# Optimization experiments

Measured on AMD Instinct MI355X. Metric: run time of the kernel, lower is better.

## Reference

```python
import jax, jax.numpy as jnp
import numpy as np

N_NODES = 50000
N_EDGES = 800000
D = 128


def setup_inputs() -> dict:
    key = jax.random.key(0)
    k1, k2, k3, k4, k5 = jax.random.split(key, 5)
    node_attr = jax.random.normal(k1, (N_NODES, D), dtype=jnp.float32)
    edge_index = jax.random.randint(k2, (2, N_EDGES), 0, N_NODES, dtype=jnp.int64)
    edge_attr = jax.random.normal(k3, (N_EDGES, D), dtype=jnp.float32)
    # 2-layer MLP: (3D -> D) -> ReLU -> (D -> D), scaled init
    w1 = jax.random.normal(k4, (3 * D, D), dtype=jnp.float32) * (1.0 / np.sqrt(3 * D))
    b1 = jnp.zeros((D,), dtype=jnp.float32)
    w2 = jax.random.normal(k5, (D, D), dtype=jnp.float32) * (1.0 / np.sqrt(D))
    b2 = jnp.zeros((D,), dtype=jnp.float32)
    return {"node_attr": node_attr, "edge_index": edge_index, "edge_attr": edge_attr,
            "w1": w1, "b1": b1, "w2": w2, "b2": b2}


def reference(node_attr, edge_index, edge_attr, w1, b1, w2, b2):
    senders_idx = edge_index[0]
    receivers_idx = edge_index[1]
    senders_attr = node_attr[senders_idx]      # [E, D] irregular gather
    receivers_attr = node_attr[receivers_idx]  # [E, D] irregular gather
    collected = jnp.concatenate([senders_attr, receivers_attr, edge_attr], axis=1)  # [E, 3D]
    h = jax.nn.relu(collected @ w1 + b1)       # [E, D]
    edge_attr_new = h @ w2 + b2                # [E, D]
    return edge_attr_new
```

## Files before the change

### kernel.cpp

```cpp
#include <hip/hip_runtime.h>


#define NE 800000
#define DD 128

typedef float f32x4v __attribute__((ext_vector_type(4)));
typedef float f32x16 __attribute__((ext_vector_type(16)));
typedef _Float16 f16x8 __attribute__((ext_vector_type(8)));
typedef _Float16 f16x4 __attribute__((ext_vector_type(4)));

__device__ __forceinline__ f16x4 cvt4(f32x4v v) {
    f16x4 r;
    r[0] = (_Float16)v[0]; r[1] = (_Float16)v[1];
    r[2] = (_Float16)v[2]; r[3] = (_Float16)v[3];
    return r;
}

__global__ void prep_w(const float* __restrict__ w1, const float* __restrict__ w2,
                       _Float16* __restrict__ w1t, _Float16* __restrict__ w2f) {
    int i = blockIdx.x * 256 + threadIdx.x;
    if (i < 384 * 128) {
        int col = i / 384;
        int k = i - col * 384;
        float v = w1[(size_t)k * 128 + col];
        int byteoff = col * 768 + ((k * 2) ^ ((col & 15) << 4));
        *(_Float16*)((char*)w1t + byteoff) = (_Float16)v;
    } else {
        int j = i - 384 * 128;
        int kk2 = j >> 10;
        int col = (j >> 3) & 127;
        int jj = j & 7;
        w2f[j] = (_Float16)w2[(size_t)(kk2 * 8 + jj) * 128 + col];
    }
}

#define MFMA_SEG(SEG)                                                                     \
    _Pragma("unroll")                                                                     \
    for (int kk8 = 0; kk8 < 8; kk8++) {                                                   \
        f16x8 a = *(const f16x8*)(ab + r31 * 256 + ((kk8 * 32 + g2 * 16) ^ xa));          \
        _Pragma("unroll")                                                                 \
        for (int n = 0; n < 4; n++) {                                                     \
            const int col = n * 32 + r31;                                                 \
            f16x8 b = *(const f16x8*)(lds + col * 768 +                                   \
                       ((((SEG) * 8 + kk8) * 32 + g2 * 16) ^ ((col & 15) << 4)));         \
            acc[n] = __builtin_amdgcn_mfma_f32_32x32x16_f16(a, b, acc[n], 0, 0, 0);       \
        }                                                                                 \
    }

#define WRITE_SEG(V)                                                                      \
    _Pragma("unroll")                                                                     \
    for (int i = 0; i < 16; i++) {                                                        \
        const int row = 2 * i + g2;                                                       \
        *(f16x4*)(ab + row * 256 + ((r31 * 8) ^ ((row & 15) << 4))) = cvt4(V[i]);         \
    }

__global__ __attribute__((amdgpu_flat_work_group_size(512, 512),
                          amdgpu_waves_per_eu(2, 2)))
void edge_mlp(
    const float* __restrict__ node_attr,
    const int* __restrict__ eidx,
    const float* __restrict__ edge_attr,
    const _Float16* __restrict__ w1t,
    const float* __restrict__ b1,
    const _Float16* __restrict__ w2f,
    const float* __restrict__ b2,
    float* __restrict__ out) {
    extern __shared__ char lds[];

    const int tid = threadIdx.x;
    const int wid = tid >> 6;
    const int lane = tid & 63;
    const int r31 = lane & 31;
    const int g2 = lane >> 5;

    {
        const char* src = (const char*)w1t;
        #pragma unroll
        for (int i = 0; i < 12; i++) {
            int off = (tid + i * 512) * 16;
            *(f16x8*)(lds + off) = *(const f16x8*)(src + off);
        }
    }

    float b1v[4], b2v[4];
    #pragma unroll
    for (int n = 0; n < 4; n++) { b1v[n] = b1[n * 32 + r31]; b2v[n] = b2[n * 32 + r31]; }

    __syncthreads();

    const int ebase = blockIdx.x * 256 + wid * 32;
    char* ab = lds + 96 * 1024 + wid * 8192;
    const int xa = (r31 & 15) << 4;

    const int sidx = eidx[ebase + r31];
    const int ridx = eidx[NE + ebase + r31];

    f32x4v sv[16];
    #pragma unroll
    for (int i = 0; i < 16; i++) {
        int r = __shfl(sidx, 2 * i + g2);
        sv[i] = *(const f32x4v*)(node_attr + (size_t)r * DD + r31 * 4);
    }
    __builtin_amdgcn_sched_barrier(0);

    WRITE_SEG(sv)

    f32x4v rv[16];
    #pragma unroll
    for (int i = 0; i < 16; i++) {
        int r = __shfl(ridx, 2 * i + g2);
        rv[i] = *(const f32x4v*)(node_attr + (size_t)r * DD + r31 * 4);
    }
    f32x4v ev[16];
    #pragma unroll
    for (int i = 0; i < 16; i++) {
        const int row = 2 * i + g2;
        ev[i] = __builtin_nontemporal_load(
            (const f32x4v*)(edge_attr + (size_t)(ebase + row) * DD + r31 * 4));
    }
    __builtin_amdgcn_sched_barrier(0);

    f32x16 acc[4] = {};
    __builtin_amdgcn_wave_barrier();

    MFMA_SEG(0)

    WRITE_SEG(rv)
    __builtin_amdgcn_wave_barrier();

    MFMA_SEG(1)

    WRITE_SEG(ev)

    f16x8 b2f[8][4];
    #pragma unroll
    for (int kk = 0; kk < 8; kk++)
        #pragma unroll
        for (int n = 0; n < 4; n++)
            b2f[kk][n] = *(const f16x8*)(w2f + ((size_t)((kk * 2 + g2) * 128 + n * 32 + r31)) * 8);
    __builtin_amdgcn_sched_barrier(0);
    __builtin_amdgcn_wave_barrier();

    MFMA_SEG(2)

    #pragma unroll
    for (int n = 0; n < 4; n++) {
        const int col = n * 32 + r31;
        #pragma unroll
        for (int reg = 0; reg < 16; reg++) {
            const int row = (reg & 3) + 8 * (reg >> 2) + 4 * g2;
            float v = fmaxf(acc[n][reg] + b1v[n], 0.0f);
            *(_Float16*)(ab + row * 256 + ((col * 2) ^ ((row & 15) << 4))) = (_Float16)v;
        }
    }
    __builtin_amdgcn_wave_barrier();

    f32x16 acc2[4] = {};
    #pragma unroll
    for (int kk = 0; kk < 8; kk++) {
        f16x8 a = *(const f16x8*)(ab + r31 * 256 + ((kk * 32 + g2 * 16) ^ xa));
        #pragma unroll
        for (int n = 0; n < 4; n++)
            acc2[n] = __builtin_amdgcn_mfma_f32_32x32x16_f16(a, b2f[kk][n], acc2[n], 0, 0, 0);
    }

    #pragma unroll
    for (int n = 0; n < 4; n++) {
        #pragma unroll
        for (int reg = 0; reg < 16; reg++) {
            const int row = (reg & 3) + 8 * (reg >> 2) + 4 * g2;
            __builtin_nontemporal_store(acc2[n][reg] + b2v[n],
                out + (size_t)(ebase + row) * DD + n * 32 + r31);
        }
    }
}

extern "C" void kernel_launch(void* const* d_in, const int* in_sizes, int n_in,
                              void* d_out, int out_size, void* d_ws, size_t ws_size,
                              hipStream_t stream) {
    const float* node_attr = (const float*)d_in[0];
    const int* eidx = (const int*)d_in[1];
    const float* edge_attr = (const float*)d_in[2];
    const float* w1 = (const float*)d_in[3];
    const float* b1 = (const float*)d_in[4];
    const float* w2 = (const float*)d_in[5];
    const float* b2 = (const float*)d_in[6];
    float* out = (float*)d_out;

    _Float16* w1t = (_Float16*)d_ws;
    _Float16* w2f = w1t + 384 * 128;

    hipFuncSetAttribute((const void*)edge_mlp,
                        hipFuncAttributeMaxDynamicSharedMemorySize, 160 * 1024);

    prep_w<<<256, 256, 0, stream>>>(w1, w2, w1t, w2f);
    edge_mlp<<<3125, 512, 160 * 1024, stream>>>(node_attr, eidx, edge_attr,
                                                w1t, b1, w2f, b2, out);
}
```

Before: 288.6 us.

## Make edge MLP kernel persistent with cross-tile prefetch of sender gathers

Launches 256 persistent blocks that loop over 32-edge wave tiles with a stride of 2048, so the W1 copy into LDS is paid once per block instead of once per 256 edges. Inside the loop, the next tile's edge indices and sender-row gathers are issued before the final MFMA segment, overlapping gather latency with compute. W2 fragments are now loaded in two halves per iteration rather than held whole, which lowers register pressure at the cost of repeated global/L2 reads. The risk is a less even load split across CUs and extra register use for the prefetched sender rows.

```diff
diff --git a/kernel.cpp b/kernel.cpp
--- a/kernel.cpp
+++ b/kernel.cpp
@@ -3,6 +3,8 @@
 
 #define NE 800000
 #define DD 128
+#define NWT 25000
+#define WSTRIDE 2048
 
 typedef float f32x4v __attribute__((ext_vector_type(4)));
 typedef float f32x16 __attribute__((ext_vector_type(16)));
@@ -88,14 +90,14 @@
 
     __syncthreads();
 
-    const int ebase = blockIdx.x * 256 + wid * 32;
     char* ab = lds + 96 * 1024 + wid * 8192;
     const int xa = (r31 & 15) << 4;
 
-    const int sidx = eidx[ebase + r31];
-    const int ridx = eidx[NE + ebase + r31];
-
-    f32x4v sv[16];
+    int g = blockIdx.x * 8 + wid;
+    int sidx = eidx[g * 32 + r31];
+    int ridx = eidx[NE + g * 32 + r31];
+
+    f32x4v sv[16], rv[16], ev[16];
     #pragma unroll
     for (int i = 0; i < 16; i++) {
         int r = __shfl(sidx, 2 * i + g2);
@@ -103,75 +105,104 @@
     }
     __builtin_amdgcn_sched_barrier(0);
 
-    WRITE_SEG(sv)
-
-    f32x4v rv[16];
-    #pragma unroll
-    for (int i = 0; i < 16; i++) {
-        int r = __shfl(ridx, 2 * i + g2);
-        rv[i] = *(const f32x4v*)(node_attr + (size_t)r * DD + r31 * 4);
-    }
-    f32x4v ev[16];
-    #pragma unroll
-    for (int i = 0; i < 16; i++) {
-        const int row = 2 * i + g2;
-        ev[i] = __builtin_nontemporal_load(
-            (const f32x4v*)(edge_attr + (size_t)(ebase + row) * DD + r31 * 4));
-    }
-    __builtin_amdgcn_sched_barrier(0);
-
-    f32x16 acc[4] = {};
-    __builtin_amdgcn_wave_barrier();
-
-    MFMA_SEG(0)
-
-    WRITE_SEG(rv)
-    __builtin_amdgcn_wave_barrier();
-
-    MFMA_SEG(1)
-
-    WRITE_SEG(ev)
-
-    f16x8 b2f[8][4];
-    #pragma unroll
-    for (int kk = 0; kk < 8; kk++)
-        #pragma unroll
-        for (int n = 0; n < 4; n++)
-            b2f[kk][n] = *(const f16x8*)(w2f + ((size_t)((kk * 2 + g2) * 128 + n * 32 + r31)) * 8);
-    __builtin_amdgcn_sched_barrier(0);
-    __builtin_amdgcn_wave_barrier();
-
-    MFMA_SEG(2)
-
-    #pragma unroll
-    for (int n = 0; n < 4; n++) {
-        const int col = n * 32 + r31;
-        #pragma unroll
-        for (int reg = 0; reg < 16; reg++) {
-            const int row = (reg & 3) + 8 * (reg >> 2) + 4 * g2;
-            float v = fmaxf(acc[n][reg] + b1v[n], 0.0f);
-            *(_Float16*)(ab + row * 256 + ((col * 2) ^ ((row & 15) << 4))) = (_Float16)v;
-        }
-    }
-    __builtin_amdgcn_wave_barrier();
-
-    f32x16 acc2[4] = {};
-    #pragma unroll
-    for (int kk = 0; kk < 8; kk++) {
-        f16x8 a = *(const f16x8*)(ab + r31 * 256 + ((kk * 32 + g2 * 16) ^ xa));
-        #pragma unroll
-        for (int n = 0; n < 4; n++)
-            acc2[n] = __builtin_amdgcn_mfma_f32_32x32x16_f16(a, b2f[kk][n], acc2[n], 0, 0, 0);
-    }
-
-    #pragma unroll
-    for (int n = 0; n < 4; n++) {
-        #pragma unroll
-        for (int reg = 0; reg < 16; reg++) {
-            const int row = (reg & 3) + 8 * (reg >> 2) + 4 * g2;
-            __builtin_nontemporal_store(acc2[n][reg] + b2v[n],
-                out + (size_t)(ebase + row) * DD + n * 32 + r31);
-        }
+    while (g < NWT) {
+        const int ebase = g * 32;
+
+        WRITE_SEG(sv)
+
+        #pragma unroll
+        for (int i = 0; i < 16; i++) {
+            int r = __shfl(ridx, 2 * i + g2);
+            rv[i] = *(const f32x4v*)(node_attr + (size_t)r * DD + r31 * 4);
+        }
+        #pragma unroll
+        for (int i = 0; i < 16; i++) {
+            const int row = 2 * i + g2;
+            ev[i] = __builtin_nontemporal_load(
+                (const f32x4v*)(edge_attr + (size_t)(ebase + row) * DD + r31 * 4));
+        }
+        __builtin_amdgcn_sched_barrier(0);
+
+        const int gn = g + WSTRIDE;
+        int sidx_n = 0, ridx_n = 0;
+        if (gn < NWT) {
+            sidx_n = eidx[gn * 32 + r31];
+            ridx_n = eidx[NE + gn * 32 + r31];
+        }
+
+        f32x16 acc[4] = {};
+        __builtin_amdgcn_wave_barrier();
+        MFMA_SEG(0)
+
+        WRITE_SEG(rv)
+        __builtin_amdgcn_wave_barrier();
+        MFMA_SEG(1)
+
+        WRITE_SEG(ev)
+        __builtin_amdgcn_wave_barrier();
+
+        if (gn < NWT) {
+            #pragma unroll
+            for (int i = 0; i < 16; i++) {
+                int r = __shfl(sidx_n, 2 * i + g2);
+                sv[i] = *(const f32x4v*)(node_attr + (size_t)r * DD + r31 * 4);
+            }
+        }
+        __builtin_amdgcn_sched_barrier(0);
+
+        MFMA_SEG(2)
+
+        #pragma unroll
+        for (int n = 0; n < 4; n++) {
+            const int col = n * 32 + r31;
+            #pragma unroll
+            for (int reg = 0; reg < 16; reg++) {
+                const int row = (reg & 3) + 8 * (reg >> 2) + 4 * g2;
+                float v = fmaxf(acc[n][reg] + b1v[n], 0.0f);
+                *(_Float16*)(ab + row * 256 + ((col * 2) ^ ((row & 15) << 4))) = (_Float16)v;
+            }
+        }
+        __builtin_amdgcn_wave_barrier();
+
+        f32x16 acc2[4] = {};
+        f16x8 b2fa[4][4];
+        #pragma unroll
+        for (int kk = 0; kk < 4; kk++)
+            #pragma unroll
+            for (int n = 0; n < 4; n++)
+                b2fa[kk][n] = *(const f16x8*)(w2f + ((size_t)((kk * 2 + g2) * 128 + n * 32 + r31)) * 8);
+        #pragma unroll
+        for (int kk = 0; kk < 4; kk++) {
+            f16x8 a = *(const f16x8*)(ab + r31 * 256 + ((kk * 32 + g2 * 16) ^ xa));
+            #pragma unroll
+            for (int n = 0; n < 4; n++)
+                acc2[n] = __builtin_amdgcn_mfma_f32_32x32x16_f16(a, b2fa[kk][n], acc2[n], 0, 0, 0);
+        }
+        f16x8 b2fb[4][4];
+        #pragma unroll
+        for (int kk = 0; kk < 4; kk++)
+            #pragma unroll
+            for (int n = 0; n < 4; n++)
+                b2fb[kk][n] = *(const f16x8*)(w2f + ((size_t)(((kk + 4) * 2 + g2) * 128 + n * 32 + r31)) * 8);
+        #pragma unroll
+        for (int kk = 4; kk < 8; kk++) {
+            f16x8 a = *(const f16x8*)(ab + r31 * 256 + ((kk * 32 + g2 * 16) ^ xa));
+            #pragma unroll
+            for (int n = 0; n < 4; n++)
+                acc2[n] = __builtin_amdgcn_mfma_f32_32x32x16_f16(a, b2fb[kk - 4][n], acc2[n], 0, 0, 0);
+        }
+
+        #pragma unroll
+        for (int n = 0; n < 4; n++) {
+            #pragma unroll
+            for (int reg = 0; reg < 16; reg++) {
+                const int row = (reg & 3) + 8 * (reg >> 2) + 4 * g2;
+                __builtin_nontemporal_store(acc2[n][reg] + b2v[n],
+                    out + (size_t)(ebase + row) * DD + n * 32 + r31);
+            }
+        }
+
+        sidx = sidx_n; ridx = ridx_n; g = gn;
     }
 }
 
@@ -194,6 +225,6 @@
                         hipFuncAttributeMaxDynamicSharedMemorySize, 160 * 1024);
 
     prep_w<<<256, 256, 0, stream>>>(w1, w2, w1t, w2f);
-    edge_mlp<<<3125, 512, 160 * 1024, stream>>>(node_attr, eidx, edge_attr,
-                                                w1t, b1, w2f, b2, out);
-}
+    edge_mlp<<<256, 512, 160 * 1024, stream>>>(node_attr, eidx, edge_attr,
+                                               w1t, b1, w2f, b2, out);
+}
```

Measured after the change: 714.0 us. 147% more time.
